# Performance work log

Hardware: AMD Instinct MI355X
Metric: run time of the kernel (lower is better)

Reference implementation:

```python
import jax, jax.numpy as jnp
import numpy as np

NUM_SPINS = 32
BATCH = 8192
HIDDEN = 1024
INPUT_DIM = 2
NUM_LAYERS = 1
EPS = 1e-12

# factorial table 0..NUM_SPINS in float32 (matches torch storing int factorials into float tensor)
_FACT = jnp.asarray(
    np.cumprod(np.concatenate([np.ones(1), np.arange(1, NUM_SPINS + 1, dtype=np.float64)])).astype(np.float32)
)


def setup_inputs() -> dict:
    key = jax.random.key(0)
    ks = jax.random.split(key, 7)
    bits = jax.random.randint(ks[0], (NUM_SPINS, BATCH), 0, 2)
    data_in = jax.nn.one_hot(bits, INPUT_DIM, dtype=jnp.float32)  # one-hot spin configs
    s = 1.0 / np.sqrt(HIDDEN)
    W_ih = jax.random.normal(ks[1], (HIDDEN, INPUT_DIM), jnp.float32) * s
    W_hh = jax.random.normal(ks[2], (HIDDEN, HIDDEN), jnp.float32) * s
    b_ih = jax.random.normal(ks[3], (HIDDEN,), jnp.float32) * s
    b_hh = jax.random.normal(ks[4], (HIDDEN,), jnp.float32) * s
    W_lin = jax.random.normal(ks[5], (INPUT_DIM, HIDDEN), jnp.float32) * s
    b_lin = jax.random.normal(ks[6], (INPUT_DIM,), jnp.float32) * s
    return {"data_in": data_in, "W_ih": W_ih, "W_hh": W_hh, "b_ih": b_ih,
            "b_hh": b_hh, "W_lin": W_lin, "b_lin": b_lin}


def _perm_w(n_idx, k):
    # n! / max(0,k)! * heaviside(k, 1)  -> 0 if k < 0, else fact ratio (1 at k==0 handled by ratio)
    k_i = jnp.clip(k, 0, NUM_SPINS).astype(jnp.int32)
    return _FACT[n_idx] / _FACT[k_i] * (k >= 0).astype(jnp.float32)


def _forward(data_in, W_ih, W_hh, b_ih, b_hh, W_lin, b_lin):
    N = NUM_SPINS
    B = data_in.shape[1]
    # shift inputs right by one spin; first input is init_state [1, 0]
    init = jnp.tile(jnp.array([1.0, 0.0], jnp.float32), (B, 1))
    data = jnp.concatenate([init[None], data_in[:-1]], axis=0)  # [N, B, 2]
    half = N // 2

    def step(carry, xs):
        h, cu, cd = carry
        x, s = xs  # x: [B, 2], s: spin index scalar
        for _ in range(NUM_LAYERS):  # same cell applied num_layers times, as in torch code
            h = jnp.tanh(x @ W_ih.T + b_ih + h @ W_hh.T + b_hh)
        p = jax.nn.softmax(h @ W_lin.T + b_lin, axis=1)  # [B, 2]
        mask = (s != 0).astype(jnp.float32)  # cum counts only updated for spin_num != 0
        cu = cu + mask * x[:, 0]
        cd = cd + mask * x[:, 1]
        up_w = _perm_w(N - s, half - cu) + EPS
        dn_w = _perm_w(N - s, half - cd) + EPS
        w = jnp.stack([up_w, dn_w], axis=1)  # [B, 2]
        p = jnp.where(s == 0, p, p * w)  # no weighting at first spin
        return (h, cu, cd), p

    h0 = jnp.zeros((B, HIDDEN), jnp.float32)
    z = jnp.zeros((B,), jnp.float32)
    _, probs = jax.lax.scan(step, (h0, z, z), (data, jnp.arange(N)))
    return probs / jnp.sum(probs, axis=2, keepdims=True)


def reference(data_in, W_ih, W_hh, b_ih, b_hh, W_lin, b_lin):
    return _forward(data_in, W_ih, W_hh, b_ih, b_hh, W_lin, b_lin)
```

## Files before the change

### kernel.cpp

```cpp
#include <hip/hip_runtime.h>


typedef __bf16 bf16;
typedef __bf16 bf16x8 __attribute__((ext_vector_type(8)));
typedef float  f32x4  __attribute__((ext_vector_type(4)));

#define HID   1024
#define BATCH 8192
#define NSPIN 32

#define AS1 __attribute__((address_space(1)))
#define AS3 __attribute__((address_space(3)))

__device__ __forceinline__ float tanh_fast(float x) {
    float ax = fabsf(x);
    float t  = __expf(-2.0f * ax);
    float r  = (1.0f - t) * __builtin_amdgcn_rcpf(1.0f + t);
    return __builtin_copysignf(r, x);
}


__global__ void prep1(const float* __restrict__ din, const float* __restrict__ Wih,
                      const float* __restrict__ Whh, const float* __restrict__ bih,
                      const float* __restrict__ bhh,
                      bf16* __restrict__ Wbf, float* __restrict__ u0, float* __restrict__ u1,
                      unsigned int* __restrict__ words, float* __restrict__ fact) {
    long idx = (long)blockIdx.x * blockDim.x + threadIdx.x;
    long stride = (long)gridDim.x * blockDim.x;
    for (long i = idx; i < (long)HID * HID; i += stride) Wbf[i] = (bf16)Whh[i];
    for (long i = idx; i < HID; i += stride) {
        u0[i] = Wih[i * 2 + 0] + bih[i] + bhh[i];
        u1[i] = Wih[i * 2 + 1] + bih[i] + bhh[i];
    }
    for (long b = idx; b < BATCH; b += stride) {
        unsigned int wv = 0;
        for (int j = 0; j < 31; ++j)
            wv |= (din[((long)j * BATCH + b) * 2 + 1] != 0.0f ? 1u : 0u) << j;
        words[b] = wv;
    }
    if (idx == 0) {
        double f = 1.0; fact[0] = 1.0f;
        for (int k = 1; k <= NSPIN; ++k) { f *= k; fact[k] = (float)f; }
    }
}

__global__ void prep2(const float* __restrict__ u0, const float* __restrict__ Wlin,
                      const float* __restrict__ blin,
                      bf16* __restrict__ hrow, float* __restrict__ l0s) {
    __shared__ float red0[16], red1[16];
    int t = threadIdx.x;
    float hv = tanh_fast(u0[t]);
    hrow[t] = (bf16)hv;
    float s0 = hv * Wlin[t], s1 = hv * Wlin[HID + t];
    #pragma unroll
    for (int off = 1; off < 64; off <<= 1) {
        s0 += __shfl_xor(s0, off, 64);
        s1 += __shfl_xor(s1, off, 64);
    }
    if ((t & 63) == 0) { red0[t >> 6] = s0; red1[t >> 6] = s1; }
    __syncthreads();
    if (t == 0) {
        float a = blin[0], b = blin[1];
        for (int i = 0; i < 16; ++i) { a += red0[i]; b += red1[i]; }
        l0s[0] = a; l0s[1] = b;
    }
}


__global__ __launch_bounds__(512, 2) void tree_step(
        const bf16* __restrict__ hin, bf16* __restrict__ hout,
        const bf16* __restrict__ Wbf,
        const float* __restrict__ u0, const float* __restrict__ u1,
        const float* __restrict__ Wlin,
        float* __restrict__ slog_s, int M) {
    __shared__ __align__(16) bf16 sA0[64 * 64];
    __shared__ __align__(16) bf16 sA1[64 * 64];
    __shared__ __align__(16) bf16 sA2[64 * 64];
    __shared__ __align__(16) bf16 sB0[128 * 64];
    __shared__ __align__(16) bf16 sB1[128 * 64];
    __shared__ __align__(16) bf16 sB2[128 * 64];

    const int tid = threadIdx.x;
    const int w = tid >> 6, l = tid & 63;
    const long rowM = (long)blockIdx.x * 64;
    const int  colPanel = blockIdx.y;
    const int  colN = colPanel * 128;
    const int wr = w >> 2, wc = w & 3;
    const int fr = l & 15, fq = l >> 4;
    const int lrow = l >> 3, lchk = l & 7;

    f32x4 acc[2][2] = {};

#define TSTG(SA, SB, KT) do {                                                                \
    {                                                                                        \
        const int r_ = w * 8 + lrow;                                                         \
        const int sc_ = (lchk ^ (r_ & 7)) * 8;                                               \
        __builtin_amdgcn_global_load_lds(                                                    \
            (const AS1 void*)(hin + (rowM + r_) * HID + (KT) * 64 + sc_),                    \
            (AS3 void*)(&SA[(w * 8) * 64]), 16, 0, 0);                                       \
    }                                                                                        \
    _Pragma("unroll")                                                                        \
    for (int i = 0; i < 2; ++i) {                                                            \
        const int r_ = w * 16 + i * 8 + lrow;                                                \
        const int sc_ = (lchk ^ (r_ & 7)) * 8;                                               \
        __builtin_amdgcn_global_load_lds(                                                    \
            (const AS1 void*)(Wbf + (long)(colN + r_) * HID + (KT) * 64 + sc_),              \
            (AS3 void*)(&SB[(w * 16 + i * 8) * 64]), 16, 0, 0);                              \
    }                                                                                        \
} while (0)

#define TBODY(CA, CB, NA, NB, T) do {                                                        \
    bf16x8 af[2][2], bf_[2][2];                                                              \
    _Pragma("unroll")                                                                        \
    for (int kk = 0; kk < 2; ++kk) {                                                         \
        _Pragma("unroll")                                                                    \
        for (int m = 0; m < 2; ++m) {                                                        \
            const int ra_ = wr * 32 + m * 16 + fr;                                           \
            af[kk][m] = *(const bf16x8*)&CA[ra_ * 64 + ((kk * 32 + fq * 8) ^ ((ra_ & 7) << 3))]; \
        }                                                                                    \
        _Pragma("unroll")                                                                    \
        for (int n = 0; n < 2; ++n) {                                                        \
            const int rb_ = wc * 32 + n * 16 + fr;                                           \
            bf_[kk][n] = *(const bf16x8*)&CB[rb_ * 64 + ((kk * 32 + fq * 8) ^ ((rb_ & 7) << 3))]; \
        }                                                                                    \
    }                                                                                        \
    if ((T) <= 13) TSTG(NA, NB, (T) + 2);                                                    \
    __builtin_amdgcn_s_setprio(1);                                                           \
    _Pragma("unroll")                                                                        \
    for (int kk = 0; kk < 2; ++kk)                                                           \
        _Pragma("unroll")                                                                    \
        for (int m = 0; m < 2; ++m)                                                          \
            _Pragma("unroll")                                                                \
            for (int n = 0; n < 2; ++n)                                                      \
                acc[m][n] = __builtin_amdgcn_mfma_f32_16x16x32_bf16(af[kk][m], bf_[kk][n], acc[m][n], 0, 0, 0); \
    __builtin_amdgcn_s_setprio(0);                                                           \
    __builtin_amdgcn_sched_barrier(0);                                                       \
    if ((T) <= 13)       asm volatile("s_waitcnt vmcnt(3)" ::: "memory");                    \
    else if ((T) == 14)  asm volatile("s_waitcnt vmcnt(0)" ::: "memory");                    \
    if ((T) <= 14) __builtin_amdgcn_s_barrier();                                             \
    __builtin_amdgcn_sched_barrier(0);                                                       \
} while (0)

    TSTG(sA0, sB0, 0);
    TSTG(sA1, sB1, 1);
    __builtin_amdgcn_sched_barrier(0);
    asm volatile("s_waitcnt vmcnt(3)" ::: "memory");
    __builtin_amdgcn_s_barrier();
    __builtin_amdgcn_sched_barrier(0);

    TBODY(sA0, sB0, sA2, sB2, 0);   TBODY(sA1, sB1, sA0, sB0, 1);
    TBODY(sA2, sB2, sA1, sB1, 2);   TBODY(sA0, sB0, sA2, sB2, 3);
    TBODY(sA1, sB1, sA0, sB0, 4);   TBODY(sA2, sB2, sA1, sB1, 5);
    TBODY(sA0, sB0, sA2, sB2, 6);   TBODY(sA1, sB1, sA0, sB0, 7);
    TBODY(sA2, sB2, sA1, sB1, 8);   TBODY(sA0, sB0, sA2, sB2, 9);
    TBODY(sA1, sB1, sA0, sB0, 10);  TBODY(sA2, sB2, sA1, sB1, 11);
    TBODY(sA0, sB0, sA2, sB2, 12);  TBODY(sA1, sB1, sA0, sB0, 13);
    TBODY(sA2, sB2, sA1, sB1, 14);  TBODY(sA0, sB0, sA2, sB2, 15);

#undef TBODY
#undef TSTG

    float u0v[2], u1v[2], wl0[2], wl1[2];
    int colg[2];
    #pragma unroll
    for (int n = 0; n < 2; ++n) {
        int c = colN + wc * 32 + n * 16 + fr;
        colg[n] = c;
        u0v[n] = u0[c]; u1v[n] = u1[c];
        wl0[n] = Wlin[c]; wl1[n] = Wlin[HID + c];
    }
    const int slot = colPanel * 4 + wc;

    #pragma unroll
    for (int m = 0; m < 2; ++m) {
        #pragma unroll
        for (int r = 0; r < 4; ++r) {
            long p = rowM + wr * 32 + m * 16 + fq * 4 + r;
            if (p < M) {
                float s00 = 0.f, s01 = 0.f, s10 = 0.f, s11 = 0.f;
                #pragma unroll
                for (int n = 0; n < 2; ++n) {
                    float z  = acc[m][n][r];
                    float h0 = tanh_fast(z + u0v[n]);
                    float h1 = tanh_fast(z + u1v[n]);
                    hout[(2 * p + 0) * HID + colg[n]] = (bf16)h0;
                    hout[(2 * p + 1) * HID + colg[n]] = (bf16)h1;
                    s00 += h0 * wl0[n]; s01 += h0 * wl1[n];
                    s10 += h1 * wl0[n]; s11 += h1 * wl1[n];
                }
                #pragma unroll
                for (int off = 1; off < 16; off <<= 1) {
                    s00 += __shfl_xor(s00, off, 16);
                    s01 += __shfl_xor(s01, off, 16);
                    s10 += __shfl_xor(s10, off, 16);
                    s11 += __shfl_xor(s11, off, 16);
                }
                if (fr == 0) {
                    *(float2*)&slog_s[(2 * p + 0) * 64 + slot * 2] = make_float2(s00, s01);
                    *(float2*)&slog_s[(2 * p + 1) * 64 + slot * 2] = make_float2(s10, s11);
                }
            }
        }
    }
}

__global__ void gatherh(const bf16* __restrict__ states, const unsigned int* __restrict__ words,
                        bf16* __restrict__ hbatch) {
    long v = (long)blockIdx.x * blockDim.x + threadIdx.x;
    const long total = (long)BATCH * 128;
    for (; v < total; v += (long)gridDim.x * blockDim.x) {
        int b = (int)(v >> 7), c = (int)(v & 127);
        unsigned int p = __brev(words[b] & 0x1FFFu) >> 19;
        ((bf16x8*)hbatch)[v] = ((const bf16x8*)states)[(long)p * 128 + c];
    }
}


__global__ __launch_bounds__(512, 2) void gemm_step(
        const bf16* __restrict__ hin, bf16* __restrict__ hout,
        const bf16* __restrict__ Wbf,
        const float* __restrict__ u0, const float* __restrict__ u1,
        const unsigned int* __restrict__ words, int sbit, int writeH,
        const float* __restrict__ Wlin,
        float* __restrict__ plog_s) {
    __shared__ __align__(16) bf16 sA0[128 * 64];
    __shared__ __align__(16) bf16 sA1[128 * 64];
    __shared__ __align__(16) bf16 sA2[128 * 64];
    __shared__ __align__(16) bf16 sB0[256 * 64];
    __shared__ __align__(16) bf16 sB1[256 * 64];
    __shared__ __align__(16) bf16 sB2[256 * 64];

    const int tid = threadIdx.x;
    const int w = tid >> 6, l = tid & 63;

    const int lin = blockIdx.y * 64 + blockIdx.x;
    const int xcd = lin & 7, jj = lin >> 3;
    const long rowM = (long)(xcd * 8 + (jj >> 2)) * 128;
    const int  by   = jj & 3;
    const int  colN = by * 256;

    const int wr = w >> 2, wc = w & 3;
    const int fr = l & 15, fq = l >> 4;

    f32x4 acc[4][4] = {};

    const int lrow = l >> 3;
    const int lchk = l & 7;

#define STG_A(SA, KT) do {                                                                   \
    _Pragma("unroll")                                                                        \
    for (int i = 0; i < 2; ++i) {                                                            \
        const int r_ = w * 16 + i * 8 + lrow;                                                \
        const int sc_ = (lchk ^ (r_ & 7)) * 8;                                               \
        __builtin_amdgcn_global_load_lds(                                                    \
            (const AS1 void*)(hin + (rowM + r_) * HID + (KT) * 64 + sc_),                    \
            (AS3 void*)(&SA[(w * 16 + i * 8) * 64]), 16, 0, 0);                              \
    }                                                                                        \
} while (0)

#define STG_B2(SB, KT, I0) do {                                                              \
    _Pragma("unroll")                                                                        \
    for (int i = (I0); i < (I0) + 2; ++i) {                                                  \
        const int r_ = w * 32 + i * 8 + lrow;                                                \
        const int sc_ = (lchk ^ (r_ & 7)) * 8;                                               \
        __builtin_amdgcn_global_load_lds(                                                    \
            (const AS1 void*)(Wbf + (long)(colN + r_) * HID + (KT) * 64 + sc_),              \
            (AS3 void*)(&SB[(w * 32 + i * 8) * 64]), 16, 0, 0);                              \
    }                                                                                        \
} while (0)

#define RD_FRAGS(AF, BF, SA, SB, KK) do {                                                    \
    _Pragma("unroll")                                                                        \
    for (int m = 0; m < 4; ++m) {                                                            \
        const int ra_ = wr * 64 + m * 16 + fr;                                               \
        AF[m] = *(const bf16x8*)&SA[ra_ * 64 + (((KK) * 32 + fq * 8) ^ ((ra_ & 7) << 3))];   \
    }                                                                                        \
    _Pragma("unroll")                                                                        \
    for (int n = 0; n < 4; ++n) {                                                            \
        const int rb_ = wc * 64 + n * 16 + fr;                                               \
        BF[n] = *(const bf16x8*)&SB[rb_ * 64 + (((KK) * 32 + fq * 8) ^ ((rb_ & 7) << 3))];   \
    }                                                                                        \
} while (0)

#define MFMA16(AF, BF) do {                                                                  \
    __builtin_amdgcn_s_setprio(1);                                                           \
    _Pragma("unroll")                                                                        \
    for (int m = 0; m < 4; ++m)                                                              \
        _Pragma("unroll")                                                                    \
        for (int n = 0; n < 4; ++n)                                                          \
            acc[m][n] = __builtin_amdgcn_mfma_f32_16x16x32_bf16(AF[m], BF[n], acc[m][n], 0, 0, 0); \
    __builtin_amdgcn_s_setprio(0);                                                           \
} while (0)

#define BODY(CA, CB, NA, NB, T) do {                                                         \
    bf16x8 afx[4], bfx[4], afy[4], bfy[4];                                                   \
    RD_FRAGS(afx, bfx, CA, CB, 0);                                                           \
    if ((T) <= 13) { STG_A(NA, (T) + 2); STG_B2(NB, (T) + 2, 0); }                           \
    MFMA16(afx, bfx);                                                                        \
    RD_FRAGS(afy, bfy, CA, CB, 1);                                                           \
    if ((T) <= 13) { STG_B2(NB, (T) + 2, 2); }                                               \
    MFMA16(afy, bfy);                                                                        \
    __builtin_amdgcn_sched_barrier(0);                                                       \
    if ((T) <= 13)       asm volatile("s_waitcnt vmcnt(6)" ::: "memory");                    \
    else if ((T) == 14)  asm volatile("s_waitcnt vmcnt(0)" ::: "memory");                    \
    if ((T) <= 14) __builtin_amdgcn_s_barrier();                                             \
    __builtin_amdgcn_sched_barrier(0);                                                       \
} while (0)

    STG_A(sA0, 0); STG_B2(sB0, 0, 0); STG_B2(sB0, 0, 2);
    STG_A(sA1, 1); STG_B2(sB1, 1, 0); STG_B2(sB1, 1, 2);
    __builtin_amdgcn_sched_barrier(0);
    asm volatile("s_waitcnt vmcnt(6)" ::: "memory");
    __builtin_amdgcn_s_barrier();
    __builtin_amdgcn_sched_barrier(0);

    BODY(sA0, sB0, sA2, sB2, 0);
    BODY(sA1, sB1, sA0, sB0, 1);
    BODY(sA2, sB2, sA1, sB1, 2);
    BODY(sA0, sB0, sA2, sB2, 3);
    BODY(sA1, sB1, sA0, sB0, 4);
    BODY(sA2, sB2, sA1, sB1, 5);
    BODY(sA0, sB0, sA2, sB2, 6);
    BODY(sA1, sB1, sA0, sB0, 7);
    BODY(sA2, sB2, sA1, sB1, 8);
    BODY(sA0, sB0, sA2, sB2, 9);
    BODY(sA1, sB1, sA0, sB0, 10);
    BODY(sA2, sB2, sA1, sB1, 11);
    BODY(sA0, sB0, sA2, sB2, 12);
    BODY(sA1, sB1, sA0, sB0, 13);
    BODY(sA2, sB2, sA1, sB1, 14);
    BODY(sA0, sB0, sA2, sB2, 15);

#undef BODY
#undef MFMA16
#undef RD_FRAGS
#undef STG_A
#undef STG_B2

    float u0v[4], u1v[4], wl0[4], wl1[4];
    int colg[4];
    #pragma unroll
    for (int n = 0; n < 4; ++n) {
        int c = colN + wc * 64 + n * 16 + fr;
        colg[n] = c;
        u0v[n] = u0[c]; u1v[n] = u1[c];
        wl0[n] = Wlin[c]; wl1[n] = Wlin[HID + c];
    }
    const int slot = by * 4 + wc;

    #pragma unroll
    for (int m = 0; m < 4; ++m) {
        #pragma unroll
        for (int r = 0; r < 4; ++r) {
            long rowg = rowM + wr * 64 + m * 16 + fq * 4 + r;
            int bt = (words[rowg] >> sbit) & 1;
            float s0 = 0.f, s1 = 0.f;
            #pragma unroll
            for (int n = 0; n < 4; ++n) {
                float z  = acc[m][n][r] + (bt ? u1v[n] : u0v[n]);
                float hv = tanh_fast(z);
                if (writeH) hout[rowg * HID + colg[n]] = (bf16)hv;
                s0 += hv * wl0[n];
                s1 += hv * wl1[n];
            }
            #pragma unroll
            for (int off = 1; off < 16; off <<= 1) {
                s0 += __shfl_xor(s0, off, 16);
                s1 += __shfl_xor(s1, off, 16);
            }
            if (fr == 0)
                *(float2*)&plog_s[rowg * 32 + slot * 2] = make_float2(s0, s1);
        }
    }
}


__global__ void finalize(const float* __restrict__ plog, const float* __restrict__ slog,
                         const float* __restrict__ l0s,
                         const float* __restrict__ blin, const unsigned int* __restrict__ words,
                         const float* __restrict__ fact, float* __restrict__ out) {
    long idx = (long)blockIdx.x * blockDim.x + threadIdx.x;
    if (idx >= (long)NSPIN * BATCH) return;
    int s = (int)(idx / BATCH), b = (int)(idx % BATCH);
    const unsigned int wv = words[b];

    float l0, l1;
    if (s == 0) { l0 = l0s[0]; l1 = l0s[1]; }
    else if (s <= 13) {
        unsigned int p = __brev(wv & ((1u << s) - 1)) >> (32 - s);
        const float* ps = slog + ((long)((1u << s) - 2) + p) * 64;
        l0 = blin[0]; l1 = blin[1];
        #pragma unroll
        for (int k = 0; k < 32; ++k) {
            l0 += ps[k * 2 + 0];
            l1 += ps[k * 2 + 1];
        }
    } else {
        l0 = blin[0]; l1 = blin[1];
        const float* ps = plog + ((long)(s - 14) * BATCH + b) * 32;
        #pragma unroll
        for (int k = 0; k < 16; ++k) {
            l0 += ps[k * 2 + 0];
            l1 += ps[k * 2 + 1];
        }
    }
    float mx = fmaxf(l0, l1);
    float e0 = __expf(l0 - mx), e1 = __expf(l1 - mx);
    float p0 = e0 / (e0 + e1), p1 = e1 / (e0 + e1);
    if (s > 0) {
        const int cd = __popc(wv & ((1u << s) - 1));
        const float cdf = (float)cd, cuf = (float)(s - cd);
        const float ku = 16.f - cuf, kd = 16.f - cdf;
        const int n = NSPIN - s;
        const int kui = (int)fminf(fmaxf(ku, 0.f), 32.f);
        const int kdi = (int)fminf(fmaxf(kd, 0.f), 32.f);
        const float wu = fact[n] / fact[kui] * (ku >= 0.f ? 1.f : 0.f) + 1e-12f;
        const float wd = fact[n] / fact[kdi] * (kd >= 0.f ? 1.f : 0.f) + 1e-12f;
        p0 *= wu; p1 *= wd;
    }
    float inv = 1.f / (p0 + p1);
    out[idx * 2 + 0] = p0 * inv;
    out[idx * 2 + 1] = p1 * inv;
}


extern "C" void kernel_launch(void* const* d_in, const int* in_sizes, int n_in,
                              void* d_out, int out_size, void* d_ws, size_t ws_size,
                              hipStream_t stream) {
    const float* din  = (const float*)d_in[0];
    const float* Wih  = (const float*)d_in[1];
    const float* Whh  = (const float*)d_in[2];
    const float* bih  = (const float*)d_in[3];
    const float* bhh  = (const float*)d_in[4];
    const float* Wlin = (const float*)d_in[5];
    const float* blin = (const float*)d_in[6];
    float* out = (float*)d_out;

    char* ws = (char*)d_ws;
    size_t o = 0;
    auto alloc = [&](size_t b) { size_t r = o; o += (b + 255) & ~(size_t)255; return r; };
    bf16*  Wbf  = (bf16*)(ws + alloc((size_t)HID * HID * 2));
    float* u0   = (float*)(ws + alloc(HID * 4));
    float* u1   = (float*)(ws + alloc(HID * 4));
    bf16*  hrow = (bf16*)(ws + alloc((size_t)64 * HID * 2));
    float* l0s  = (float*)(ws + alloc(2 * 4));
    float* fact = (float*)(ws + alloc(33 * 4));
    unsigned int* words = (unsigned int*)(ws + alloc((size_t)BATCH * 4));
    bf16*  hA   = (bf16*)(ws + alloc((size_t)BATCH * HID * 2));
    bf16*  hB   = (bf16*)(ws + alloc((size_t)BATCH * HID * 2));
    float* slog = (float*)(ws + alloc(((size_t)(1 << 14) - 2) * 64 * 4));
    float* plog = (float*)(ws + alloc(18L * BATCH * 32 * 4));

    prep1<<<1024, 256, 0, stream>>>(din, Wih, Whh, bih, bhh, Wbf, u0, u1, words, fact);
    prep2<<<1, 1024, 0, stream>>>(u0, Wlin, blin, hrow, l0s);

    const bf16* tin = hrow;
    bf16* tout = hA;
    for (int i = 1; i <= 13; ++i) {
        int Min = 1 << (i - 1);
        dim3 g(Min < 64 ? 1 : Min / 64, 8);
        tree_step<<<g, 512, 0, stream>>>(
            tin, tout, Wbf, u0, u1, Wlin,
            slog + ((long)(1 << i) - 2) * 64, Min);
        tin = tout;
        tout = (tout == hA) ? hB : hA;
    }
    gatherh<<<2048, 256, 0, stream>>>(tin, words, tout);

    bf16* hin = tout;
    bf16* hout = (tout == hA) ? hB : hA;
    for (int s = 14; s <= 31; ++s) {
        gemm_step<<<dim3(64, 4), 512, 0, stream>>>(
            hin, hout, Wbf, u0, u1, words, s - 1, (s < 31) ? 1 : 0, Wlin,
            plog + (size_t)(s - 14) * BATCH * 32);
        bf16* t = hin; hin = hout; hout = t;
    }
    finalize<<<(NSPIN * BATCH) / 256, 256, 0, stream>>>(plog, slog, l0s, blin, words, fact, out);
}
```

Measured before the change: 623.8 us.

## Fuse prefix-state gather into first GEMM step via precomputed row indices

Removes the gatherh kernel. Each batch's tree-state row index is precomputed in prep1, and the first gemm_step loads its A tiles indirectly through that index, which saves a full 16 MB copy and one launch. The XCD-aware block-to-tile remapping is also replaced by a plain blockIdx mapping, which may change L2 locality across XCDs.

```diff
diff --git a/kernel.cpp b/kernel.cpp
--- a/kernel.cpp
+++ b/kernel.cpp
@@ -24,7 +24,8 @@
                       const float* __restrict__ Whh, const float* __restrict__ bih,
                       const float* __restrict__ bhh,
                       bf16* __restrict__ Wbf, float* __restrict__ u0, float* __restrict__ u1,
-                      unsigned int* __restrict__ words, float* __restrict__ fact) {
+                      unsigned int* __restrict__ words, unsigned int* __restrict__ pidx,
+                      float* __restrict__ fact) {
     long idx = (long)blockIdx.x * blockDim.x + threadIdx.x;
     long stride = (long)gridDim.x * blockDim.x;
     for (long i = idx; i < (long)HID * HID; i += stride) Wbf[i] = (bf16)Whh[i];
@@ -37,6 +38,7 @@
         for (int j = 0; j < 31; ++j)
             wv |= (din[((long)j * BATCH + b) * 2 + 1] != 0.0f ? 1u : 0u) << j;
         words[b] = wv;
+        pidx[b] = __brev(wv & 0x1FFFu) >> 19;
     }
     if (idx == 0) {
         double f = 1.0; fact[0] = 1.0f;
@@ -204,23 +206,13 @@
     }
 }
 
-__global__ void gatherh(const bf16* __restrict__ states, const unsigned int* __restrict__ words,
-                        bf16* __restrict__ hbatch) {
-    long v = (long)blockIdx.x * blockDim.x + threadIdx.x;
-    const long total = (long)BATCH * 128;
-    for (; v < total; v += (long)gridDim.x * blockDim.x) {
-        int b = (int)(v >> 7), c = (int)(v & 127);
-        unsigned int p = __brev(words[b] & 0x1FFFu) >> 19;
-        ((bf16x8*)hbatch)[v] = ((const bf16x8*)states)[(long)p * 128 + c];
-    }
-}
-
 
 __global__ __launch_bounds__(512, 2) void gemm_step(
         const bf16* __restrict__ hin, bf16* __restrict__ hout,
         const bf16* __restrict__ Wbf,
         const float* __restrict__ u0, const float* __restrict__ u1,
-        const unsigned int* __restrict__ words, int sbit, int writeH,
+        const unsigned int* __restrict__ words,
+        const unsigned int* __restrict__ pidx, int sbit, int writeH,
         const float* __restrict__ Wlin,
         float* __restrict__ plog_s) {
     __shared__ __align__(16) bf16 sA0[128 * 64];
@@ -232,11 +224,8 @@
 
     const int tid = threadIdx.x;
     const int w = tid >> 6, l = tid & 63;
-
-    const int lin = blockIdx.y * 64 + blockIdx.x;
-    const int xcd = lin & 7, jj = lin >> 3;
-    const long rowM = (long)(xcd * 8 + (jj >> 2)) * 128;
-    const int  by   = jj & 3;
+    const long rowM = (long)blockIdx.x * 128;
+    const int  by   = blockIdx.y;
     const int  colN = by * 256;
 
     const int wr = w >> 2, wc = w & 3;
@@ -247,14 +236,24 @@
     const int lrow = l >> 3;
     const int lchk = l & 7;
 
+    long arow0 = rowM + w * 16 + 0 + lrow;
+    long arow1 = rowM + w * 16 + 8 + lrow;
+    if (pidx) { arow0 = pidx[arow0]; arow1 = pidx[arow1]; }
+
 #define STG_A(SA, KT) do {                                                                   \
-    _Pragma("unroll")                                                                        \
-    for (int i = 0; i < 2; ++i) {                                                            \
-        const int r_ = w * 16 + i * 8 + lrow;                                                \
+    {                                                                                        \
+        const int r_ = w * 16 + 0 + lrow;                                                    \
         const int sc_ = (lchk ^ (r_ & 7)) * 8;                                               \
         __builtin_amdgcn_global_load_lds(                                                    \
-            (const AS1 void*)(hin + (rowM + r_) * HID + (KT) * 64 + sc_),                    \
-            (AS3 void*)(&SA[(w * 16 + i * 8) * 64]), 16, 0, 0);                              \
+            (const AS1 void*)(hin + arow0 * HID + (KT) * 64 + sc_),                          \
+            (AS3 void*)(&SA[(w * 16 + 0) * 64]), 16, 0, 0);                                  \
+    }                                                                                        \
+    {                                                                                        \
+        const int r_ = w * 16 + 8 + lrow;                                                    \
+        const int sc_ = (lchk ^ (r_ & 7)) * 8;                                               \
+        __builtin_amdgcn_global_load_lds(                                                    \
+            (const AS1 void*)(hin + arow1 * HID + (KT) * 64 + sc_),                          \
+            (AS3 void*)(&SA[(w * 16 + 8) * 64]), 16, 0, 0);                                  \
     }                                                                                        \
 } while (0)
 
@@ -446,12 +445,13 @@
     float* l0s  = (float*)(ws + alloc(2 * 4));
     float* fact = (float*)(ws + alloc(33 * 4));
     unsigned int* words = (unsigned int*)(ws + alloc((size_t)BATCH * 4));
+    unsigned int* pidx  = (unsigned int*)(ws + alloc((size_t)BATCH * 4));
     bf16*  hA   = (bf16*)(ws + alloc((size_t)BATCH * HID * 2));
     bf16*  hB   = (bf16*)(ws + alloc((size_t)BATCH * HID * 2));
     float* slog = (float*)(ws + alloc(((size_t)(1 << 14) - 2) * 64 * 4));
     float* plog = (float*)(ws + alloc(18L * BATCH * 32 * 4));
 
-    prep1<<<1024, 256, 0, stream>>>(din, Wih, Whh, bih, bhh, Wbf, u0, u1, words, fact);
+    prep1<<<1024, 256, 0, stream>>>(din, Wih, Whh, bih, bhh, Wbf, u0, u1, words, pidx, fact);
     prep2<<<1, 1024, 0, stream>>>(u0, Wlin, blin, hrow, l0s);
 
     const bf16* tin = hrow;
@@ -465,13 +465,13 @@
         tin = tout;
         tout = (tout == hA) ? hB : hA;
     }
-    gatherh<<<2048, 256, 0, stream>>>(tin, words, tout);
-
-    bf16* hin = tout;
-    bf16* hout = (tout == hA) ? hB : hA;
+    bf16* hin = (bf16*)tin;
+    bf16* hout = (tin == hA) ? hB : hA;
     for (int s = 14; s <= 31; ++s) {
         gemm_step<<<dim3(64, 4), 512, 0, stream>>>(
-            hin, hout, Wbf, u0, u1, words, s - 1, (s < 31) ? 1 : 0, Wlin,
+            hin, hout, Wbf, u0, u1, words,
+            (s == 14) ? pidx : (const unsigned int*)nullptr,
+            s - 1, (s < 31) ? 1 : 0, Wlin,
             plog + (size_t)(s - 14) * BATCH * 32);
         bf16* t = hin; hin = hout; hout = t;
     }
```

New measurement: 608.7 us. 1.02x faster.
